# Kernel tuning notes

Measured on AMD Instinct MI355X. Metric: run time of the kernel, lower is better.

Reference implementation:

```python
import jax, jax.numpy as jnp
import numpy as np


def setup_inputs() -> dict:
    key = jax.random.key(0)
    k1, k2 = jax.random.split(key)
    # x: [B, D, H, W, C] 3D latent grid, C == embedding_dim
    x = jax.random.normal(k1, (4, 32, 32, 16, 256), dtype=jnp.float32)
    # codebook stored as (embedding_dim, num_embeddings) like the TF variable
    embeddings = jax.random.uniform(k2, (256, 4096), dtype=jnp.float32)
    return {"x": x, "embeddings": embeddings}


def reference(x, embeddings):
    # Inference-mode forward of VectorQuantizer.call (training=False).
    D, K = embeddings.shape  # (embedding_dim, num_embeddings)
    flat = x.reshape(-1, D)  # [N, D]
    # squared L2 distances: ||z||^2 + ||e||^2 - 2 z.e  -> [N, K]
    sim = flat @ embeddings
    dist = (jnp.sum(flat * flat, axis=1, keepdims=True)
            + jnp.sum(embeddings * embeddings, axis=0)
            - 2.0 * sim)
    idx = jnp.argmin(dist, axis=1)  # [N]
    # nearest-codebook lookup (gather codebook columns)
    quantized = jnp.take(embeddings.T, idx, axis=0).reshape(x.shape)
    # perplexity from code usage histogram (avoids materializing [N,K] one-hot)
    n = flat.shape[0]
    counts = jnp.zeros((K,), dtype=jnp.float32).at[idx].add(1.0)
    avg_probs = counts / n
    perplexity = jnp.exp(-jnp.sum(avg_probs * jnp.log(avg_probs + 1e-10)))
    return quantized, perplexity
```

## Files before the change

### kernel.cpp

```cpp
#include <hip/hip_runtime.h>
#include <hip/hip_bf16.h>

#define NROWS 65536
#define DIM   256
#define KCB   4096
#define CHUNK 32
#define NCH   (KCB / CHUNK)
#define NBUF  4
#define BUFB  16384
#define NENH_BASE (NBUF * BUFB)

typedef __attribute__((ext_vector_type(8))) short bf16x8;
typedef __attribute__((ext_vector_type(4))) float f32x4;

#define WAITV0  asm volatile("s_waitcnt vmcnt(0)" ::: "memory")
#define WAITV8  asm volatile("s_waitcnt vmcnt(8)" ::: "memory")
#define WAITV16 asm volatile("s_waitcnt vmcnt(16)" ::: "memory")

__device__ inline short f2bf(float f) {
    __hip_bfloat16 h = __float2bfloat16(f);
    return *reinterpret_cast<short*>(&h);
}

__global__ void prep_transpose(const float* __restrict__ E,
                               float* __restrict__ ET32,
                               ushort* __restrict__ ETbf)
{
    __shared__ float tile[64][65];
    const int kb = blockIdx.x * 64;
    const int db = blockIdx.y * 64;
    const int lo = threadIdx.x & 63;
    const int hi = threadIdx.x >> 6;

#pragma unroll
    for (int i = 0; i < 16; ++i) {
        int d = i * 4 + hi;
        tile[lo][d] = E[(size_t)(db + d) * KCB + kb + lo];
    }
    __syncthreads();
#pragma unroll
    for (int i = 0; i < 16; ++i) {
        int k = i * 4 + hi;
        float v = tile[k][lo];
        size_t off = (size_t)(kb + k) * DIM + db + lo;
        ET32[off] = v;
        ETbf[off] = (ushort)f2bf(v);
    }
}

__global__ void prep_enorm(const float* __restrict__ E, float* __restrict__ nenh)
{
    int k = blockIdx.x * 256 + threadIdx.x;
    float s = 0.0f;
#pragma unroll 8
    for (int d = 0; d < DIM; ++d) {
        float v = E[(size_t)d * KCB + k];
        s = fmaf(v, v, s);
    }
    nenh[k] = -0.5f * s;
}

__shared__ char lds_raw[NBUF * BUFB + 16384];

template <int BUF>
__device__ __forceinline__ void stage_chunk(
    const char* __restrict__ etb, const int (&soff)[8], int wave, int ct)
{
    const char* base = etb + (size_t)ct * (CHUNK * 512);
#pragma unroll
    for (int j = 0; j < 8; ++j) {
        __builtin_amdgcn_global_load_lds(
            (const __attribute__((address_space(1))) unsigned*)(base + soff[j]),
            (__attribute__((address_space(3))) unsigned*)
                (lds_raw + BUF * BUFB + wave * 8192 + j * 1024),
            16, 0, 0);
    }
}

template <int BUF, int TC>
__device__ __forceinline__ void read_batch(
    const int (&boffB)[8], int nhbyte, bf16x8 (&bfr)[8], float& nh)
{
#pragma unroll
    for (int kc = 0; kc < 8; ++kc)
        bfr[kc] = *(const bf16x8*)(lds_raw + BUF * BUFB + TC * 8192 + boffB[kc]);
    nh = *(const float*)(lds_raw + NENH_BASE + nhbyte);
}

__device__ __forceinline__ void mfma_cluster(
    const bf16x8 (&afrag)[4][8], const bf16x8 (&bfr)[8], float nh,
    float (&best)[4][4], int (&bidx)[4][4], int col)
{
    f32x4 acc[4];
#pragma unroll
    for (int rt = 0; rt < 4; ++rt) acc[rt] = {nh, nh, nh, nh};
    __builtin_amdgcn_s_setprio(1);
#pragma unroll
    for (int kc = 0; kc < 8; ++kc)
#pragma unroll
        for (int rt = 0; rt < 4; ++rt)
            acc[rt] = __builtin_amdgcn_mfma_f32_16x16x32_bf16(
                afrag[rt][kc], bfr[kc], acc[rt], 0, 0, 0);
    __builtin_amdgcn_s_setprio(0);
#pragma unroll
    for (int rt = 0; rt < 4; ++rt)
#pragma unroll
        for (int r = 0; r < 4; ++r) {
            float s = acc[rt][r];
            bool gt = s > best[rt][r];
            bidx[rt][r] = gt ? col : bidx[rt][r];
            best[rt][r] = fmaxf(best[rt][r], s);
        }
}

template <int BUF, int WN, bool STG, bool RA>
__device__ __forceinline__ void chunk_step(
    const char* __restrict__ etb, const int (&soff)[8], int wave, int ct,
    const int (&boffB)[8], int l15,
    const bf16x8 (&afrag)[4][8],
    bf16x8 (&bA)[8], bf16x8 (&bB)[8], float& nhA, float& nhB,
    float (&best)[4][4], int (&bidx)[4][4])
{
    if constexpr (WN == 8) { WAITV8; } else { WAITV0; }
    __builtin_amdgcn_s_barrier();
    __builtin_amdgcn_sched_barrier(0);
    if constexpr (STG) stage_chunk<(BUF + 3) & 3>(etb, soff, wave, ct + 3);
    read_batch<BUF, 1>(boffB, ct * 128 + 64 + l15 * 4, bB, nhB);
    mfma_cluster(afrag, bA, nhA, best, bidx, ct * CHUNK + l15);
    if constexpr (RA)
        read_batch<(BUF + 1) & 3, 0>(boffB, (ct + 1) * 128 + l15 * 4, bA, nhA);
    mfma_cluster(afrag, bB, nhB, best, bidx, ct * CHUNK + 16 + l15);
}

__global__ __launch_bounds__(128, 1)
void vq_argmin(const float* __restrict__ X,
               const ushort* __restrict__ ETbf,
               const float* __restrict__ nenh,
               int* __restrict__ idxout)
{
    const int tid  = threadIdx.x;
    const int lane = tid & 63;
    const int wave = tid >> 6;
    const int l15  = lane & 15;
    const int g    = lane >> 4;
    const int m    = l15 & 7;
    const long rowbase = (long)blockIdx.x * 128 + wave * 64;
    const char* etb = (const char*)ETbf;

    bf16x8 afrag[4][8];
#pragma unroll
    for (int rt = 0; rt < 4; ++rt) {
        const float* xr = X + (rowbase + rt * 16 + l15) * DIM;
#pragma unroll
        for (int kc = 0; kc < 8; ++kc) {
            int k0 = g * 64 + kc * 8;
            float4 v0 = *(const float4*)(xr + k0);
            float4 v1 = *(const float4*)(xr + k0 + 4);
            bf16x8 f;
            f[0] = f2bf(v0.x); f[1] = f2bf(v0.y);
            f[2] = f2bf(v0.z); f[3] = f2bf(v0.w);
            f[4] = f2bf(v1.x); f[5] = f2bf(v1.y);
            f[6] = f2bf(v1.z); f[7] = f2bf(v1.w);
            afrag[rt][kc] = f;
        }
    }

    int soff[8];
#pragma unroll
    for (int j = 0; j < 8; ++j) {
        const int o    = wave * 8192 + j * 1024 + lane * 16;
        const int col0 = o >> 9;
        const int cph  = (o >> 4) & 31;
        soff[j] = (col0 << 9) + ((cph ^ (col0 & 7)) << 4);
    }

    int boffB[8];
#pragma unroll
    for (int kc = 0; kc < 8; ++kc)
        boffB[kc] = l15 * 512 + ((((g << 3) + kc) ^ m) << 4);

#pragma unroll
    for (int j = 0; j < 8; ++j) {
        int o = wave * 8192 + j * 1024 + lane * 16;
        __builtin_amdgcn_global_load_lds(
            (const __attribute__((address_space(1))) unsigned*)((const char*)nenh + o),
            (__attribute__((address_space(3))) unsigned*)
                (lds_raw + NENH_BASE + wave * 8192 + j * 1024),
            16, 0, 0);
    }
    stage_chunk<0>(etb, soff, wave, 0);
    stage_chunk<1>(etb, soff, wave, 1);
    stage_chunk<2>(etb, soff, wave, 2);

    float best[4][4];
    int   bidx[4][4];
#pragma unroll
    for (int rt = 0; rt < 4; ++rt)
#pragma unroll
        for (int r = 0; r < 4; ++r) { best[rt][r] = -3.4e38f; bidx[rt][r] = 0x7fffffff; }

    bf16x8 bA[8], bB[8];
    float nhA, nhB;

    WAITV16;
    __builtin_amdgcn_s_barrier();
    __builtin_amdgcn_sched_barrier(0);
    read_batch<0, 0>(boffB, 0 + l15 * 4, bA, nhA);

    for (int gq = 0; gq < 31; ++gq) {
        const int ct = gq * 4;
        chunk_step<0, 8, true, true>(etb, soff, wave, ct + 0, boffB, l15,
                                     afrag, bA, bB, nhA, nhB, best, bidx);
        chunk_step<1, 8, true, true>(etb, soff, wave, ct + 1, boffB, l15,
                                     afrag, bA, bB, nhA, nhB, best, bidx);
        chunk_step<2, 8, true, true>(etb, soff, wave, ct + 2, boffB, l15,
                                     afrag, bA, bB, nhA, nhB, best, bidx);
        chunk_step<3, 8, true, true>(etb, soff, wave, ct + 3, boffB, l15,
                                     afrag, bA, bB, nhA, nhB, best, bidx);
    }
    chunk_step<0, 8, true,  true >(etb, soff, wave, 124, boffB, l15,
                                   afrag, bA, bB, nhA, nhB, best, bidx);
    chunk_step<1, 8, false, true >(etb, soff, wave, 125, boffB, l15,
                                   afrag, bA, bB, nhA, nhB, best, bidx);
    chunk_step<2, 0, false, true >(etb, soff, wave, 126, boffB, l15,
                                   afrag, bA, bB, nhA, nhB, best, bidx);
    chunk_step<3, 0, false, false>(etb, soff, wave, 127, boffB, l15,
                                   afrag, bA, bB, nhA, nhB, best, bidx);

#pragma unroll
    for (int rt = 0; rt < 4; ++rt) {
#pragma unroll
        for (int r = 0; r < 4; ++r) {
            float v = best[rt][r];
            int   ix = bidx[rt][r];
#pragma unroll
            for (int off = 1; off < 16; off <<= 1) {
                float ov = __shfl_xor(v, off, 64);
                int   oi = __shfl_xor(ix, off, 64);
                if (ov > v || (ov == v && oi < ix)) { v = ov; ix = oi; }
            }
            if (l15 == 0) {
                long row = rowbase + rt * 16 + g * 4 + r;
                idxout[row] = ix;
            }
        }
    }
}

__global__ void vq_gather(const int* __restrict__ idxin,
                          const float* __restrict__ ET32,
                          float* __restrict__ out,
                          unsigned* __restrict__ counts)
{
    const int tid = threadIdx.x;
    const long n  = (long)blockIdx.x * 4 + (tid >> 6);
    const int d4  = tid & 63;
    const int idx = idxin[n];
    float4 v = *(const float4*)(ET32 + (size_t)idx * DIM + d4 * 4);
    *(float4*)(out + n * DIM + d4 * 4) = v;
    if (d4 == 0) atomicAdd(&counts[idx], 1u);
}

__global__ void vq_perplexity(const unsigned* __restrict__ counts, float* __restrict__ outp)
{
    __shared__ float wsum[4];
    const int tid = threadIdx.x;
    float s = 0.0f;
    for (int k = tid; k < KCB; k += 256) {
        float p = (float)counts[k] * (1.0f / (float)NROWS);
        s += p * logf(p + 1e-10f);
    }
#pragma unroll
    for (int off = 32; off >= 1; off >>= 1) s += __shfl_down(s, off, 64);
    if ((tid & 63) == 0) wsum[tid >> 6] = s;
    __syncthreads();
    if (tid == 0) outp[0] = expf(-(wsum[0] + wsum[1] + wsum[2] + wsum[3]));
}

extern "C" void kernel_launch(void* const* d_in, const int* in_sizes, int n_in,
                              void* d_out, int out_size, void* d_ws, size_t ws_size,
                              hipStream_t stream)
{
    const float* X = (const float*)d_in[0];
    const float* E = (const float*)d_in[1];
    float* out = (float*)d_out;

    char* ws = (char*)d_ws;
    float*    ET32   = (float*)ws;
    ushort*   ETbf   = (ushort*)(ws + (size_t)KCB * DIM * 4);
    float*    nenh   = (float*)(ws + (size_t)KCB * DIM * 6);
    int*      idxbuf = (int*)(ws + (size_t)KCB * DIM * 6 + KCB * 4);
    unsigned* counts = (unsigned*)(ws + (size_t)KCB * DIM * 6 + KCB * 4 + NROWS * 4);

    hipMemsetAsync(counts, 0, KCB * sizeof(unsigned), stream);

    prep_transpose<<<dim3(KCB / 64, DIM / 64), dim3(256), 0, stream>>>(E, ET32, ETbf);
    prep_enorm<<<KCB / 256, dim3(256), 0, stream>>>(E, nenh);
    vq_argmin<<<NROWS / 128, dim3(128), 0, stream>>>(X, ETbf, nenh, idxbuf);
    vq_gather<<<NROWS / 4, dim3(256), 0, stream>>>(idxbuf, ET32, out, counts);
    vq_perplexity<<<1, dim3(256), 0, stream>>>(counts, out + (size_t)NROWS * DIM);
}
```

Measured before the change: 205.4 us.

## Split codebook columns across 8 waves per block and merge argmin in LDS

The argmin kernel grows from 2 waves covering 128 rows to 8 waves covering 256 rows. Four row groups are each split into two column halves, so each wave processes 16 codebook columns per chunk instead of 32. Staging of each chunk is spread across all 8 waves, and the two half-results are merged through LDS at the end. The aim is more waves per CU and shared codebook staging to hide latency and cut global traffic per row. The cost is an extra LDS reduction step and a per-chunk barrier across more waves, with two blocks per CU.

```diff
diff --git a/kernel.cpp b/kernel.cpp
--- a/kernel.cpp
+++ b/kernel.cpp
@@ -13,9 +13,9 @@
 typedef __attribute__((ext_vector_type(8))) short bf16x8;
 typedef __attribute__((ext_vector_type(4))) float f32x4;
 
-#define WAITV0  asm volatile("s_waitcnt vmcnt(0)" ::: "memory")
-#define WAITV8  asm volatile("s_waitcnt vmcnt(8)" ::: "memory")
-#define WAITV16 asm volatile("s_waitcnt vmcnt(16)" ::: "memory")
+#define WAITV0 asm volatile("s_waitcnt vmcnt(0)" ::: "memory")
+#define WAITV2 asm volatile("s_waitcnt vmcnt(2)" ::: "memory")
+#define WAITV4 asm volatile("s_waitcnt vmcnt(4)" ::: "memory")
 
 __device__ inline short f2bf(float f) {
     __hip_bfloat16 h = __float2bfloat16(f);
@@ -64,26 +64,26 @@
 
 template <int BUF>
 __device__ __forceinline__ void stage_chunk(
-    const char* __restrict__ etb, const int (&soff)[8], int wave, int ct)
+    const char* __restrict__ etb, const int (&soff)[2], int wave, int ct)
 {
     const char* base = etb + (size_t)ct * (CHUNK * 512);
 #pragma unroll
-    for (int j = 0; j < 8; ++j) {
+    for (int j = 0; j < 2; ++j) {
         __builtin_amdgcn_global_load_lds(
             (const __attribute__((address_space(1))) unsigned*)(base + soff[j]),
             (__attribute__((address_space(3))) unsigned*)
-                (lds_raw + BUF * BUFB + wave * 8192 + j * 1024),
+                (lds_raw + BUF * BUFB + wave * 2048 + j * 1024),
             16, 0, 0);
     }
 }
 
-template <int BUF, int TC>
+template <int BUF>
 __device__ __forceinline__ void read_batch(
     const int (&boffB)[8], int nhbyte, bf16x8 (&bfr)[8], float& nh)
 {
 #pragma unroll
     for (int kc = 0; kc < 8; ++kc)
-        bfr[kc] = *(const bf16x8*)(lds_raw + BUF * BUFB + TC * 8192 + boffB[kc]);
+        bfr[kc] = *(const bf16x8*)(lds_raw + BUF * BUFB + boffB[kc]);
     nh = *(const float*)(lds_raw + NENH_BASE + nhbyte);
 }
 
@@ -115,24 +115,22 @@
 
 template <int BUF, int WN, bool STG, bool RA>
 __device__ __forceinline__ void chunk_step(
-    const char* __restrict__ etb, const int (&soff)[8], int wave, int ct,
-    const int (&boffB)[8], int l15,
+    const char* __restrict__ etb, const int (&soff)[2], int wave, int ct,
+    const int (&boffB)[8], int hc,
     const bf16x8 (&afrag)[4][8],
-    bf16x8 (&bA)[8], bf16x8 (&bB)[8], float& nhA, float& nhB,
+    bf16x8 (&cur)[8], float& nhc, bf16x8 (&nxt)[8], float& nhn,
     float (&best)[4][4], int (&bidx)[4][4])
 {
-    if constexpr (WN == 8) { WAITV8; } else { WAITV0; }
+    if constexpr (WN == 2) { WAITV2; } else { WAITV0; }
     __builtin_amdgcn_s_barrier();
     __builtin_amdgcn_sched_barrier(0);
     if constexpr (STG) stage_chunk<(BUF + 3) & 3>(etb, soff, wave, ct + 3);
-    read_batch<BUF, 1>(boffB, ct * 128 + 64 + l15 * 4, bB, nhB);
-    mfma_cluster(afrag, bA, nhA, best, bidx, ct * CHUNK + l15);
     if constexpr (RA)
-        read_batch<(BUF + 1) & 3, 0>(boffB, (ct + 1) * 128 + l15 * 4, bA, nhA);
-    mfma_cluster(afrag, bB, nhB, best, bidx, ct * CHUNK + 16 + l15);
-}
-
-__global__ __launch_bounds__(128, 1)
+        read_batch<(BUF + 1) & 3>(boffB, (ct + 1) * 128 + hc * 4, nxt, nhn);
+    mfma_cluster(afrag, cur, nhc, best, bidx, ct * CHUNK + hc);
+}
+
+__global__ __launch_bounds__(512, 2)
 void vq_argmin(const float* __restrict__ X,
                const ushort* __restrict__ ETbf,
                const float* __restrict__ nenh,
@@ -141,10 +139,13 @@
     const int tid  = threadIdx.x;
     const int lane = tid & 63;
     const int wave = tid >> 6;
+    const int rg   = wave & 3;
+    const int h    = wave >> 2;
     const int l15  = lane & 15;
     const int g    = lane >> 4;
     const int m    = l15 & 7;
-    const long rowbase = (long)blockIdx.x * 128 + wave * 64;
+    const int hc   = h * 16 + l15;
+    const long rowbase = (long)blockIdx.x * 256 + rg * 64;
     const char* etb = (const char*)ETbf;
 
     bf16x8 afrag[4][8];
@@ -165,10 +166,10 @@
         }
     }
 
-    int soff[8];
-#pragma unroll
-    for (int j = 0; j < 8; ++j) {
-        const int o    = wave * 8192 + j * 1024 + lane * 16;
+    int soff[2];
+#pragma unroll
+    for (int j = 0; j < 2; ++j) {
+        const int o    = wave * 2048 + j * 1024 + lane * 16;
         const int col0 = o >> 9;
         const int cph  = (o >> 4) & 31;
         soff[j] = (col0 << 9) + ((cph ^ (col0 & 7)) << 4);
@@ -177,15 +178,15 @@
     int boffB[8];
 #pragma unroll
     for (int kc = 0; kc < 8; ++kc)
-        boffB[kc] = l15 * 512 + ((((g << 3) + kc) ^ m) << 4);
-
-#pragma unroll
-    for (int j = 0; j < 8; ++j) {
-        int o = wave * 8192 + j * 1024 + lane * 16;
+        boffB[kc] = h * 8192 + l15 * 512 + ((((g << 3) + kc) ^ m) << 4);
+
+#pragma unroll
+    for (int j = 0; j < 2; ++j) {
+        int o = wave * 2048 + j * 1024 + lane * 16;
         __builtin_amdgcn_global_load_lds(
             (const __attribute__((address_space(1))) unsigned*)((const char*)nenh + o),
             (__attribute__((address_space(3))) unsigned*)
-                (lds_raw + NENH_BASE + wave * 8192 + j * 1024),
+                (lds_raw + NENH_BASE + wave * 2048 + j * 1024),
             16, 0, 0);
     }
     stage_chunk<0>(etb, soff, wave, 0);
@@ -202,31 +203,32 @@
     bf16x8 bA[8], bB[8];
     float nhA, nhB;
 
-    WAITV16;
+    WAITV4;
     __builtin_amdgcn_s_barrier();
     __builtin_amdgcn_sched_barrier(0);
-    read_batch<0, 0>(boffB, 0 + l15 * 4, bA, nhA);
+    read_batch<0>(boffB, hc * 4, bA, nhA);
 
     for (int gq = 0; gq < 31; ++gq) {
         const int ct = gq * 4;
-        chunk_step<0, 8, true, true>(etb, soff, wave, ct + 0, boffB, l15,
-                                     afrag, bA, bB, nhA, nhB, best, bidx);
-        chunk_step<1, 8, true, true>(etb, soff, wave, ct + 1, boffB, l15,
-                                     afrag, bA, bB, nhA, nhB, best, bidx);
-        chunk_step<2, 8, true, true>(etb, soff, wave, ct + 2, boffB, l15,
-                                     afrag, bA, bB, nhA, nhB, best, bidx);
-        chunk_step<3, 8, true, true>(etb, soff, wave, ct + 3, boffB, l15,
-                                     afrag, bA, bB, nhA, nhB, best, bidx);
-    }
-    chunk_step<0, 8, true,  true >(etb, soff, wave, 124, boffB, l15,
-                                   afrag, bA, bB, nhA, nhB, best, bidx);
-    chunk_step<1, 8, false, true >(etb, soff, wave, 125, boffB, l15,
-                                   afrag, bA, bB, nhA, nhB, best, bidx);
-    chunk_step<2, 0, false, true >(etb, soff, wave, 126, boffB, l15,
-                                   afrag, bA, bB, nhA, nhB, best, bidx);
-    chunk_step<3, 0, false, false>(etb, soff, wave, 127, boffB, l15,
-                                   afrag, bA, bB, nhA, nhB, best, bidx);
-
+        chunk_step<0, 2, true, true>(etb, soff, wave, ct + 0, boffB, hc,
+                                     afrag, bA, nhA, bB, nhB, best, bidx);
+        chunk_step<1, 2, true, true>(etb, soff, wave, ct + 1, boffB, hc,
+                                     afrag, bB, nhB, bA, nhA, best, bidx);
+        chunk_step<2, 2, true, true>(etb, soff, wave, ct + 2, boffB, hc,
+                                     afrag, bA, nhA, bB, nhB, best, bidx);
+        chunk_step<3, 2, true, true>(etb, soff, wave, ct + 3, boffB, hc,
+                                     afrag, bB, nhB, bA, nhA, best, bidx);
+    }
+    chunk_step<0, 2, true,  true >(etb, soff, wave, 124, boffB, hc,
+                                   afrag, bA, nhA, bB, nhB, best, bidx);
+    chunk_step<1, 2, false, true >(etb, soff, wave, 125, boffB, hc,
+                                   afrag, bB, nhB, bA, nhA, best, bidx);
+    chunk_step<2, 0, false, true >(etb, soff, wave, 126, boffB, hc,
+                                   afrag, bA, nhA, bB, nhB, best, bidx);
+    chunk_step<3, 0, false, false>(etb, soff, wave, 127, boffB, hc,
+                                   afrag, bB, nhB, bA, nhA, best, bidx);
+
+    __syncthreads();
 #pragma unroll
     for (int rt = 0; rt < 4; ++rt) {
 #pragma unroll
@@ -240,10 +242,20 @@
                 if (ov > v || (ov == v && oi < ix)) { v = ov; ix = oi; }
             }
             if (l15 == 0) {
-                long row = rowbase + rt * 16 + g * 4 + r;
-                idxout[row] = ix;
+                int row = rg * 64 + rt * 16 + g * 4 + r;
+                *(float*)(lds_raw + h * 1024 + row * 4) = v;
+                *(int*)(lds_raw + 2048 + h * 1024 + row * 4) = ix;
             }
         }
+    }
+    __syncthreads();
+    if (tid < 256) {
+        float b0 = *(const float*)(lds_raw + tid * 4);
+        float b1 = *(const float*)(lds_raw + 1024 + tid * 4);
+        int   i0 = *(const int*)(lds_raw + 2048 + tid * 4);
+        int   i1 = *(const int*)(lds_raw + 3072 + tid * 4);
+        bool take1 = (b1 > b0) || (b1 == b0 && i1 < i0);
+        idxout[(long)blockIdx.x * 256 + tid] = take1 ? i1 : i0;
     }
 }
 
@@ -296,7 +308,7 @@
 
     prep_transpose<<<dim3(KCB / 64, DIM / 64), dim3(256), 0, stream>>>(E, ET32, ETbf);
     prep_enorm<<<KCB / 256, dim3(256), 0, stream>>>(E, nenh);
-    vq_argmin<<<NROWS / 128, dim3(128), 0, stream>>>(X, ETbf, nenh, idxbuf);
+    vq_argmin<<<NROWS / 256, dim3(512), 0, stream>>>(X, ETbf, nenh, idxbuf);
     vq_gather<<<NROWS / 4, dim3(256), 0, stream>>>(idxbuf, ET32, out, counts);
     vq_perplexity<<<1, dim3(256), 0, stream>>>(counts, out + (size_t)NROWS * DIM);
 }
```

New measurement: 287.4 us. 1.4x slower.
